# Performance work log

Measured on AMD Instinct MI355X. Metric: run time of the kernel, lower is better.

## Reference

```python
import jax, jax.numpy as jnp
import numpy as np

S, D, H, F = 4096, 1024, 16, 4096
DH = D // H  # 64
EPS = 1e-6


def _layer_norm(x, scale, bias):
    mu = jnp.mean(x, axis=-1, keepdims=True)
    var = jnp.mean(jnp.square(x - mu), axis=-1, keepdims=True)
    return (x - mu) * jax.lax.rsqrt(var + EPS) * scale + bias


def setup_inputs() -> dict:
    key = jax.random.key(0)
    ks = jax.random.split(key, 12)
    s = 0.02
    return {
        "x": jax.random.normal(ks[0], (S, D), jnp.float32),
        "Wq": jax.random.normal(ks[1], (D, H, DH), jnp.float32) * s,
        "bq": jnp.zeros((H, DH), jnp.float32),
        "Wk": jax.random.normal(ks[2], (D, H, DH), jnp.float32) * s,
        "bk": jnp.zeros((H, DH), jnp.float32),
        "Wv": jax.random.normal(ks[3], (D, H, DH), jnp.float32) * s,
        "bv": jnp.zeros((H, DH), jnp.float32),
        "Wo": jax.random.normal(ks[4], (H, DH, D), jnp.float32) * s,
        "bo": jnp.zeros((D,), jnp.float32),
        "ln1_scale": jnp.ones((D,), jnp.float32),
        "ln1_bias": jnp.zeros((D,), jnp.float32),
        "ln2_scale": jnp.ones((D,), jnp.float32),
        "ln2_bias": jnp.zeros((D,), jnp.float32),
        "W1": jax.random.normal(ks[5], (D, F), jnp.float32) * s,
        "b1": jnp.zeros((F,), jnp.float32),
        "W2": jax.random.normal(ks[6], (F, D), jnp.float32) * s,
        "b2": jnp.zeros((D,), jnp.float32),
    }


def reference(x, Wq, bq, Wk, bk, Wv, bv, Wo, bo,
              ln1_scale, ln1_bias, ln2_scale, ln2_bias,
              W1, b1, W2, b2):
    # --- attention block (pre-LN, no mask, no dropout, no RoPE) ---
    y = _layer_norm(x, ln1_scale, ln1_bias)            # [S, D]
    q = jnp.einsum("sd,dhk->shk", y, Wq) + bq          # [S, H, DH]
    k = jnp.einsum("sd,dhk->shk", y, Wk) + bk
    v = jnp.einsum("sd,dhk->shk", y, Wv) + bv
    scale = jnp.float32(1.0 / np.sqrt(DH))
    scores = jnp.einsum("qhd,khd->hqk", q * scale, k)  # [H, S, S]
    w = jax.nn.softmax(scores, axis=-1)
    ctx = jnp.einsum("hqk,khd->qhd", w, v)             # [S, H, DH]
    attn_out = jnp.einsum("qhd,hdo->qo", ctx, Wo) + bo  # [S, D]
    x = x + attn_out
    # --- FFN block ---
    y = _layer_norm(x, ln2_scale, ln2_bias)
    y = jax.nn.gelu(y @ W1 + b1, approximate=False)
    y = y @ W2 + b2
    return x + y
```

## Files before the change

### kernel.cpp

```cpp
#include <hip/hip_runtime.h>
#include <cstdint>
#include <cstddef>


typedef __attribute__((ext_vector_type(8))) __bf16 bf16x8;
typedef __attribute__((ext_vector_type(4))) float f32x4;
typedef __attribute__((ext_vector_type(2))) float f32x2;
typedef __attribute__((ext_vector_type(16))) float f32x16;
typedef __attribute__((ext_vector_type(4))) unsigned int u32x4;

__device__ inline unsigned short f2bf(float f) {
  unsigned int u = __float_as_uint(f);
  u += 0x7fffu + ((u >> 16) & 1u);
  return (unsigned short)(u >> 16);
}

__device__ inline void gload_lds16(const unsigned short* g, unsigned short* l) {
  __builtin_amdgcn_global_load_lds(
      (const __attribute__((address_space(1))) void*)g,
      (__attribute__((address_space(3))) void*)l, 16, 0, 0);
}

__global__ __launch_bounds__(256) void transpose_cvt(const float* __restrict__ in,
                                                     unsigned short* __restrict__ out,
                                                     int K, int N) {
  __shared__ float t[32][33];
  int nb = blockIdx.x * 32, kb = blockIdx.y * 32;
  int tx = threadIdx.x & 31, ty = threadIdx.x >> 5;
#pragma unroll
  for (int i = 0; i < 32; i += 8)
    t[ty + i][tx] = in[(size_t)(kb + ty + i) * N + nb + tx];
  __syncthreads();
#pragma unroll
  for (int i = 0; i < 32; i += 8)
    out[(size_t)(nb + ty + i) * K + kb + tx] = f2bf(t[tx][ty + i]);
}

__global__ __launch_bounds__(256) void concat3(const float* __restrict__ a,
                                               const float* __restrict__ b,
                                               const float* __restrict__ c,
                                               float* __restrict__ out) {
  int i = blockIdx.x * 256 + threadIdx.x;
  float v = (i < 1024) ? a[i] : (i < 2048 ? b[i - 1024] : c[i - 2048]);
  out[i] = v;
}

__global__ __launch_bounds__(256) void ln_kernel(const float* __restrict__ x,
                                                 const float* __restrict__ gamma,
                                                 const float* __restrict__ beta,
                                                 unsigned short* __restrict__ y) {
  int row = blockIdx.x, tid = threadIdx.x;
  const float4 v = ((const float4*)(x + (size_t)row * 1024))[tid];
  float s = v.x + v.y + v.z + v.w;
#pragma unroll
  for (int off = 1; off < 64; off <<= 1) s += __shfl_xor(s, off);
  __shared__ float red1[4], red2[4];
  int wave = tid >> 6;
  if ((tid & 63) == 0) red1[wave] = s;
  __syncthreads();
  float mu = (red1[0] + red1[1] + red1[2] + red1[3]) * (1.0f / 1024.0f);
  float dx = v.x - mu, dy = v.y - mu, dz = v.z - mu, dw = v.w - mu;
  float s2 = dx * dx + dy * dy + dz * dz + dw * dw;
#pragma unroll
  for (int off = 1; off < 64; off <<= 1) s2 += __shfl_xor(s2, off);
  if ((tid & 63) == 0) red2[wave] = s2;
  __syncthreads();
  float var = (red2[0] + red2[1] + red2[2] + red2[3]) * (1.0f / 1024.0f);
  float inv = rsqrtf(var + 1e-6f);
  int c = tid * 4;
  ushort4 o;
  o.x = f2bf(dx * inv * gamma[c + 0] + beta[c + 0]);
  o.y = f2bf(dy * inv * gamma[c + 1] + beta[c + 1]);
  o.z = f2bf(dz * inv * gamma[c + 2] + beta[c + 2]);
  o.w = f2bf(dw * inv * gamma[c + 3] + beta[c + 3]);
  ((ushort4*)(y + (size_t)row * 1024))[tid] = o;
}

template <bool GELU, bool RES, bool OUTBF, bool SCALEQ>
__global__ __launch_bounds__(512, 2) void gemm8(
    const unsigned short* __restrict__ A,
    const unsigned short* __restrict__ BT,
    const float* __restrict__ bias,
    const float* __restrict__ res,
    void* __restrict__ out,
    int M, int N, int K) {
  constexpr int SLOT = 512 * 64;
  __shared__ unsigned short lds[2 * SLOT];
  (void)M;

  const int nbn = N / 256;
  const int bid = blockIdx.x;
  const int cpx = (int)gridDim.x >> 3;
  const int swzb = (bid & 7) * cpx + (bid >> 3);
  const int bm = swzb / nbn, bn = swzb % nbn;
  const int tid = threadIdx.x;
  const int lane = tid & 63, quad = lane >> 4, l16 = lane & 15;
  const int wm = tid >> 8, wn = (tid >> 6) & 3;

  const int rs = tid >> 3;
  const int xo = ((tid & 7) ^ (rs & 7)) * 8;
  const unsigned short* aSrc = A + (size_t)(bm * 256 + rs) * K + xo;
  const unsigned short* bSrc = BT + (size_t)(bn * 256 + rs) * K + xo;

  const int sw0 = (quad ^ (l16 & 7)) * 8;
  const int sw1 = ((quad ^ 4) ^ (l16 & 7)) * 8;
  const int aBase = (wm * 128 + l16) * 64;
  const int bBase = 16384 + (wn * 64 + l16) * 64;

  f32x4 acc[8][4];
  const f32x4 z4 = {0.f, 0.f, 0.f, 0.f};
#pragma unroll
  for (int i = 0; i < 8; ++i)
#pragma unroll
    for (int n = 0; n < 4; ++n) acc[i][n] = z4;

  const int NT = K >> 6;
  {
    unsigned short* dA = lds + (size_t)tid * 8;
    unsigned short* dB = lds + 16384 + (size_t)tid * 8;
#pragma unroll
    for (int u = 0; u < 4; ++u) gload_lds16(aSrc + (size_t)u * 64 * K, dA + u * 4096);
#pragma unroll
    for (int u = 0; u < 4; ++u) gload_lds16(bSrc + (size_t)u * 64 * K, dB + u * 4096);
  }

  for (int j = 0; j < NT; ++j) {
    const int s = j & 1;
    asm volatile("s_waitcnt vmcnt(0) lgkmcnt(0)" ::: "memory");
    __builtin_amdgcn_s_barrier();
    __builtin_amdgcn_sched_barrier(0);
    const unsigned short* Ts = lds + s * SLOT;
    unsigned short* stA = lds + (s ^ 1) * SLOT + (size_t)tid * 8;
    unsigned short* stB = stA + 16384;
    const bool pre = (j + 1 < NT);
    const int kN = (j + 1) << 6;

    bf16x8 af[4][2], bfr[4][2];
#pragma unroll
    for (int mm = 0; mm < 4; ++mm) {
      af[mm][0] = *(const bf16x8*)(Ts + aBase + mm * 1024 + sw0);
      af[mm][1] = *(const bf16x8*)(Ts + aBase + mm * 1024 + sw1);
    }
#pragma unroll
    for (int nn = 0; nn < 2; ++nn) {
      bfr[nn][0] = *(const bf16x8*)(Ts + bBase + nn * 1024 + sw0);
      bfr[nn][1] = *(const bf16x8*)(Ts + bBase + nn * 1024 + sw1);
    }
    if (pre) {
#pragma unroll
      for (int u = 0; u < 4; ++u)
        gload_lds16(aSrc + (size_t)u * 64 * K + kN, stA + u * 4096);
#pragma unroll
      for (int u = 0; u < 4; ++u)
        gload_lds16(bSrc + (size_t)u * 64 * K + kN, stB + u * 4096);
    }
    __builtin_amdgcn_s_barrier();
    __builtin_amdgcn_s_setprio(1);
#pragma unroll
    for (int mm = 0; mm < 4; ++mm)
#pragma unroll
      for (int nn = 0; nn < 2; ++nn) {
        acc[mm][nn] = __builtin_amdgcn_mfma_f32_16x16x32_bf16(af[mm][0], bfr[nn][0], acc[mm][nn], 0, 0, 0);
        acc[mm][nn] = __builtin_amdgcn_mfma_f32_16x16x32_bf16(af[mm][1], bfr[nn][1], acc[mm][nn], 0, 0, 0);
      }
    __builtin_amdgcn_s_setprio(0);
#pragma unroll
    for (int nn = 2; nn < 4; ++nn) {
      bfr[nn][0] = *(const bf16x8*)(Ts + bBase + nn * 1024 + sw0);
      bfr[nn][1] = *(const bf16x8*)(Ts + bBase + nn * 1024 + sw1);
    }
    __builtin_amdgcn_s_barrier();
    __builtin_amdgcn_s_setprio(1);
#pragma unroll
    for (int mm = 0; mm < 4; ++mm)
#pragma unroll
      for (int nn = 2; nn < 4; ++nn) {
        acc[mm][nn] = __builtin_amdgcn_mfma_f32_16x16x32_bf16(af[mm][0], bfr[nn][0], acc[mm][nn], 0, 0, 0);
        acc[mm][nn] = __builtin_amdgcn_mfma_f32_16x16x32_bf16(af[mm][1], bfr[nn][1], acc[mm][nn], 0, 0, 0);
      }
    __builtin_amdgcn_s_setprio(0);
#pragma unroll
    for (int mm = 0; mm < 4; ++mm) {
      af[mm][0] = *(const bf16x8*)(Ts + aBase + 4096 + mm * 1024 + sw0);
      af[mm][1] = *(const bf16x8*)(Ts + aBase + 4096 + mm * 1024 + sw1);
    }
    __builtin_amdgcn_s_barrier();
    __builtin_amdgcn_s_setprio(1);
#pragma unroll
    for (int mm = 0; mm < 4; ++mm)
#pragma unroll
      for (int nn = 0; nn < 2; ++nn) {
        acc[4 + mm][nn] = __builtin_amdgcn_mfma_f32_16x16x32_bf16(af[mm][0], bfr[nn][0], acc[4 + mm][nn], 0, 0, 0);
        acc[4 + mm][nn] = __builtin_amdgcn_mfma_f32_16x16x32_bf16(af[mm][1], bfr[nn][1], acc[4 + mm][nn], 0, 0, 0);
      }
    __builtin_amdgcn_s_setprio(0);
    __builtin_amdgcn_s_barrier();
    __builtin_amdgcn_s_setprio(1);
#pragma unroll
    for (int mm = 0; mm < 4; ++mm)
#pragma unroll
      for (int nn = 2; nn < 4; ++nn) {
        acc[4 + mm][nn] = __builtin_amdgcn_mfma_f32_16x16x32_bf16(af[mm][0], bfr[nn][0], acc[4 + mm][nn], 0, 0, 0);
        acc[4 + mm][nn] = __builtin_amdgcn_mfma_f32_16x16x32_bf16(af[mm][1], bfr[nn][1], acc[4 + mm][nn], 0, 0, 0);
      }
    __builtin_amdgcn_s_setprio(0);
  }

#pragma unroll
  for (int mi = 0; mi < 8; ++mi) {
    const int row0 = bm * 256 + wm * 128 + mi * 16 + quad * 4;
#pragma unroll
    for (int ni = 0; ni < 4; ++ni) {
      const int col = bn * 256 + wn * 64 + ni * 16 + l16;
      const float bv = bias[col];
      const float qs = (SCALEQ && col < 1024) ? 0.18033688f : 1.0f;
#pragma unroll
      for (int r = 0; r < 4; ++r) {
        float v = (acc[mi][ni][r] + bv) * qs;
        if (GELU) v = 0.5f * v * (1.0f + erff(v * 0.70710678118654752440f));
        if (RES) v += res[(size_t)(row0 + r) * N + col];
        if (OUTBF)
          ((unsigned short*)out)[(size_t)(row0 + r) * N + col] = f2bf(v);
        else
          ((float*)out)[(size_t)(row0 + r) * N + col] = v;
      }
    }
  }
}

template <bool GELU, bool RES, bool OUTBF>
__global__ __launch_bounds__(512, 2) void gemm3s(
    const unsigned short* __restrict__ A,
    const unsigned short* __restrict__ BT,
    const float* __restrict__ bias,
    const float* __restrict__ res,
    void* __restrict__ out,
    int M, int N, int K) {
  constexpr int SLOT = 256 * 64;
  __shared__ unsigned short lds[3 * SLOT];
  (void)M;

  const int nbn = N / 128;
  const int bid = blockIdx.x;
  const int cpx = (int)gridDim.x >> 3;
  const int swzb = (bid & 7) * cpx + (bid >> 3);
  const int bm = swzb / nbn, bn = swzb % nbn;
  const int tid = threadIdx.x;
  const int lane = tid & 63, quad = lane >> 4, l16 = lane & 15;
  const int wm = tid >> 8, wn = (tid >> 6) & 3;

  const int rs = tid >> 3;
  const int xo = ((tid & 7) ^ (rs & 7)) * 8;
  const unsigned short* aSrc = A + (size_t)(bm * 128 + rs) * K + xo;
  const unsigned short* bSrc = BT + (size_t)(bn * 128 + rs) * K + xo;

  const int sw0 = (quad ^ (l16 & 7)) * 8;
  const int sw1 = ((quad ^ 4) ^ (l16 & 7)) * 8;
  const int aBase = (wm * 64 + l16) * 64;
  const int bBase = 8192 + (wn * 32 + l16) * 64;

  f32x4 acc[4][2];
  const f32x4 z4 = {0.f, 0.f, 0.f, 0.f};
#pragma unroll
  for (int i = 0; i < 4; ++i)
#pragma unroll
    for (int n = 0; n < 2; ++n) acc[i][n] = z4;

  const int NT = K >> 6;
  {
    unsigned short* d0 = lds + (size_t)tid * 8;
    gload_lds16(aSrc, d0);
    gload_lds16(aSrc + (size_t)64 * K, d0 + 4096);
    gload_lds16(bSrc, d0 + 8192);
    gload_lds16(bSrc + (size_t)64 * K, d0 + 8192 + 4096);
    if (NT > 1) {
      unsigned short* d1 = lds + SLOT + (size_t)tid * 8;
      gload_lds16(aSrc + 64, d1);
      gload_lds16(aSrc + (size_t)64 * K + 64, d1 + 4096);
      gload_lds16(bSrc + 64, d1 + 8192);
      gload_lds16(bSrc + (size_t)64 * K + 64, d1 + 8192 + 4096);
    }
  }

  int sl = 0;
  for (int j = 0; j < NT; ++j) {
    if (j + 1 < NT)
      asm volatile("s_waitcnt vmcnt(4) lgkmcnt(0)" ::: "memory");
    else
      asm volatile("s_waitcnt vmcnt(0) lgkmcnt(0)" ::: "memory");
    __builtin_amdgcn_s_barrier();
    __builtin_amdgcn_sched_barrier(0);
    const unsigned short* Ts = lds + sl * SLOT;
    const int sl2 = (sl >= 1) ? sl - 1 : 2;
    unsigned short* st = lds + sl2 * SLOT + (size_t)tid * 8;

    bf16x8 af[2][2], bfr[2][2];
#pragma unroll
    for (int mm = 0; mm < 2; ++mm) {
      af[mm][0] = *(const bf16x8*)(Ts + aBase + mm * 1024 + sw0);
      af[mm][1] = *(const bf16x8*)(Ts + aBase + mm * 1024 + sw1);
    }
#pragma unroll
    for (int nn = 0; nn < 2; ++nn) {
      bfr[nn][0] = *(const bf16x8*)(Ts + bBase + nn * 1024 + sw0);
      bfr[nn][1] = *(const bf16x8*)(Ts + bBase + nn * 1024 + sw1);
    }
    if (j + 2 < NT) {
      const int kN = (j + 2) << 6;
      gload_lds16(aSrc + kN, st);
      gload_lds16(aSrc + (size_t)64 * K + kN, st + 4096);
      gload_lds16(bSrc + kN, st + 8192);
      gload_lds16(bSrc + (size_t)64 * K + kN, st + 8192 + 4096);
    }
    __builtin_amdgcn_s_barrier();
    __builtin_amdgcn_s_setprio(1);
#pragma unroll
    for (int mm = 0; mm < 2; ++mm)
#pragma unroll
      for (int nn = 0; nn < 2; ++nn) {
        acc[mm][nn] = __builtin_amdgcn_mfma_f32_16x16x32_bf16(af[mm][0], bfr[nn][0], acc[mm][nn], 0, 0, 0);
        acc[mm][nn] = __builtin_amdgcn_mfma_f32_16x16x32_bf16(af[mm][1], bfr[nn][1], acc[mm][nn], 0, 0, 0);
      }
    __builtin_amdgcn_s_setprio(0);
#pragma unroll
    for (int mm = 0; mm < 2; ++mm) {
      af[mm][0] = *(const bf16x8*)(Ts + aBase + 2048 + mm * 1024 + sw0);
      af[mm][1] = *(const bf16x8*)(Ts + aBase + 2048 + mm * 1024 + sw1);
    }
    __builtin_amdgcn_s_barrier();
    __builtin_amdgcn_s_setprio(1);
#pragma unroll
    for (int mm = 0; mm < 2; ++mm)
#pragma unroll
      for (int nn = 0; nn < 2; ++nn) {
        acc[2 + mm][nn] = __builtin_amdgcn_mfma_f32_16x16x32_bf16(af[mm][0], bfr[nn][0], acc[2 + mm][nn], 0, 0, 0);
        acc[2 + mm][nn] = __builtin_amdgcn_mfma_f32_16x16x32_bf16(af[mm][1], bfr[nn][1], acc[2 + mm][nn], 0, 0, 0);
      }
    __builtin_amdgcn_s_setprio(0);
    sl = (sl == 2) ? 0 : sl + 1;
  }

#pragma unroll
  for (int mi = 0; mi < 4; ++mi) {
    const int row0 = bm * 128 + wm * 64 + mi * 16 + quad * 4;
#pragma unroll
    for (int ni = 0; ni < 2; ++ni) {
      const int col = bn * 128 + wn * 32 + ni * 16 + l16;
      const float bv = bias[col];
#pragma unroll
      for (int r = 0; r < 4; ++r) {
        float v = acc[mi][ni][r] + bv;
        if (GELU) v = 0.5f * v * (1.0f + erff(v * 0.70710678118654752440f));
        if (RES) v += res[(size_t)(row0 + r) * N + col];
        if (OUTBF)
          ((unsigned short*)out)[(size_t)(row0 + r) * N + col] = f2bf(v);
        else
          ((float*)out)[(size_t)(row0 + r) * N + col] = v;
      }
    }
  }
}

__global__ __launch_bounds__(256) void prep_kv(const unsigned short* __restrict__ qkv,
                                               unsigned short* __restrict__ Kp,
                                               unsigned short* __restrict__ Vp) {
  __shared__ unsigned short Vt[64 * 64];
  int t = blockIdx.x, h = blockIdx.y;
  int tid = threadIdx.x;
  const int r2 = tid >> 3, c0 = (tid & 7) * 8;
  size_t tb = ((size_t)h * 64 + t) * 4096;
  {
    const unsigned short* kp = qkv + (size_t)(t * 64 + r2) * 3072 + 1024 + h * 64 + c0;
    uint4 k0 = *(const uint4*)kp;
    uint4 k1 = *(const uint4*)(kp + (size_t)32 * 3072);
    int c = c0 >> 3;
    *(uint4*)(Kp + tb + c * 512 + r2 * 8) = k0;
    *(uint4*)(Kp + tb + c * 512 + (r2 + 32) * 8) = k1;
  }
  {
    const unsigned short* vp = qkv + (size_t)(t * 64 + 2 * r2) * 3072 + 2048 + h * 64 + c0;
    uint4 v0 = *(const uint4*)vp;
    uint4 v1 = *(const uint4*)(vp + 3072);
    const unsigned short* p0 = (const unsigned short*)&v0;
    const unsigned short* p1 = (const unsigned short*)&v1;
#pragma unroll
    for (int dd = 0; dd < 8; dd++) {
      unsigned int pk = (unsigned int)p0[dd] | ((unsigned int)p1[dd] << 16);
      *(unsigned int*)&Vt[(c0 + dd) * 64 + 2 * r2] = pk;
    }
  }
  __syncthreads();
#pragma unroll
  for (int u0 = 0; u0 < 2; u0++) {
    int u = tid + u0 * 256;
    *(uint4*)(Vp + tb + u * 8) = *(const uint4*)&Vt[(u & 63) * 64 + (u >> 6) * 8];
  }
}

#define ATTN_STEP(KF, VF, KN, VN, T)                                                  \
  {                                                                                   \
    f32x16 accS;                                                                      \
    _Pragma("unroll")                                                                 \
    for (int r = 0; r < 16; r++) accS[r] = 0.f;                                       \
    _Pragma("unroll")                                                                 \
    for (int kk = 0; kk < 4; kk++)                                                    \
      accS = __builtin_amdgcn_mfma_f32_32x32x16_bf16(KF[kk], qf[kk], accS, 0, 0, 0);  \
    if ((T) < 63) {                                                                   \
      const unsigned short* kt = kB + (size_t)((T) + 1) * 4096;                       \
      const unsigned short* vt = vB + (size_t)((T) + 1) * 4096;                       \
      _Pragma("unroll")                                                               \
      for (int kk = 0; kk < 4; kk++) KN[kk] = *(const bf16x8*)(kt + kk * 1024);       \
      VN[0] = *(const bf16x8*)(vt);                                                   \
      VN[1] = *(const bf16x8*)(vt + 1024);                                            \
      VN[2] = *(const bf16x8*)(vt + 256);                                             \
      VN[3] = *(const bf16x8*)(vt + 1024 + 256);                                      \
    }                                                                                 \
    unsigned int pd[8];                                                               \
    _Pragma("unroll")                                                                 \
    for (int i = 0; i < 8; i++) {                                                     \
      float a = __builtin_amdgcn_exp2f(accS[2 * i]);                                  \
      float b = __builtin_amdgcn_exp2f(accS[2 * i + 1]);                              \
      f32x2 ab = {a, b};                                                              \
      lp2 += ab;                                                                      \
      pd[i] = __builtin_amdgcn_perm(__float_as_uint(b), __float_as_uint(a), 0x07060302); \
    }                                                                                 \
    asm("v_permlane32_swap_b32 %0, %1" : "+v"(pd[0]), "+v"(pd[2]));                   \
    asm("v_permlane32_swap_b32 %0, %1" : "+v"(pd[1]), "+v"(pd[3]));                   \
    asm("v_permlane32_swap_b32 %0, %1" : "+v"(pd[4]), "+v"(pd[6]));                   \
    asm("v_permlane32_swap_b32 %0, %1" : "+v"(pd[5]), "+v"(pd[7]));                   \
    u32x4 f0 = {pd[0], pd[1], pd[2], pd[3]};                                          \
    u32x4 f1 = {pd[4], pd[5], pd[6], pd[7]};                                          \
    bf16x8 pa0 = __builtin_bit_cast(bf16x8, f0);                                      \
    bf16x8 pa1 = __builtin_bit_cast(bf16x8, f1);                                      \
    accO0 = __builtin_amdgcn_mfma_f32_32x32x16_bf16(pa0, VF[0], accO0, 0, 0, 0);      \
    accO1 = __builtin_amdgcn_mfma_f32_32x32x16_bf16(pa0, VF[2], accO1, 0, 0, 0);      \
    accO0 = __builtin_amdgcn_mfma_f32_32x32x16_bf16(pa1, VF[1], accO0, 0, 0, 0);      \
    accO1 = __builtin_amdgcn_mfma_f32_32x32x16_bf16(pa1, VF[3], accO1, 0, 0, 0);      \
  }

__global__ __launch_bounds__(256, 3) void attn_kernel(const unsigned short* __restrict__ qkv,
                                                      const unsigned short* __restrict__ Kp,
                                                      const unsigned short* __restrict__ Vp,
                                                      unsigned short* __restrict__ ctx) {
  __shared__ float comb[2 * 32 * 64];
  __shared__ float lpart[4 * 32];
  int qt = blockIdx.x, h = blockIdx.y;
  int tid = threadIdx.x;
  int w = tid >> 6, lane = tid & 63;
  int l31 = lane & 31, hi = lane >> 5;
  int qsub = w & 1, kvh = w >> 1;

  bf16x8 qf[4];
  {
    const unsigned short* qp = qkv + (size_t)(qt * 64 + qsub * 32 + l31) * 3072 + h * 64 + hi * 8;
#pragma unroll
    for (int kk = 0; kk < 4; kk++) qf[kk] = *(const bf16x8*)(qp + kk * 16);
  }

  const size_t hb = (size_t)h * 64 * 4096;
  const unsigned short* kB = Kp + hb + hi * 512 + (kvh * 32 + l31) * 8;
  const unsigned short* vB = Vp + hb + (kvh * 4 + hi) * 512 + l31 * 8;

  f32x16 accO0, accO1;
  f32x2 lp2 = {0.f, 0.f};
#pragma unroll
  for (int r = 0; r < 16; r++) { accO0[r] = 0.f; accO1[r] = 0.f; }

  bf16x8 kfa[4], vfa[4], kfb[4], vfb[4];
#pragma unroll
  for (int kk = 0; kk < 4; kk++) kfa[kk] = *(const bf16x8*)(kB + kk * 1024);
  vfa[0] = *(const bf16x8*)(vB);
  vfa[1] = *(const bf16x8*)(vB + 1024);
  vfa[2] = *(const bf16x8*)(vB + 256);
  vfa[3] = *(const bf16x8*)(vB + 1024 + 256);

  for (int t = 0; t < 64; t += 2) {
    ATTN_STEP(kfa, vfa, kfb, vfb, t);
    ATTN_STEP(kfb, vfb, kfa, vfa, t + 1);
  }

  float lp = lp2.x + lp2.y;
  lp += __shfl_xor(lp, 32);
  if (hi == 0) lpart[(kvh * 2 + qsub) * 32 + l31] = lp;
  if (kvh == 1) {
#pragma unroll
    for (int r = 0; r < 16; r++) {
      int q = (r & 3) + 8 * (r >> 2) + 4 * hi;
      comb[(qsub * 32 + q) * 64 + l31] = accO0[r];
      comb[(qsub * 32 + q) * 64 + 32 + l31] = accO1[r];
    }
  }
  __syncthreads();
  if (kvh == 0) {
#pragma unroll
    for (int r = 0; r < 16; r++) {
      int q = (r & 3) + 8 * (r >> 2) + 4 * hi;
      float l = lpart[qsub * 32 + q] + lpart[(2 + qsub) * 32 + q];
      float inv = 1.0f / l;
      float v0 = (accO0[r] + comb[(qsub * 32 + q) * 64 + l31]) * inv;
      float v1 = (accO1[r] + comb[(qsub * 32 + q) * 64 + 32 + l31]) * inv;
      int row = qt * 64 + qsub * 32 + q;
      size_t o = (size_t)row * 1024 + h * 64;
      ctx[o + l31] = f2bf(v0);
      ctx[o + 32 + l31] = f2bf(v1);
    }
  }
}

extern "C" void kernel_launch(void* const* d_in, const int* in_sizes, int n_in,
                              void* d_out, int out_size, void* d_ws, size_t ws_size,
                              hipStream_t stream) {
  const float* x   = (const float*)d_in[0];
  const float* Wq  = (const float*)d_in[1];
  const float* bq  = (const float*)d_in[2];
  const float* Wk  = (const float*)d_in[3];
  const float* bk  = (const float*)d_in[4];
  const float* Wv  = (const float*)d_in[5];
  const float* bv  = (const float*)d_in[6];
  const float* Wo  = (const float*)d_in[7];
  const float* bo  = (const float*)d_in[8];
  const float* g1  = (const float*)d_in[9];
  const float* be1 = (const float*)d_in[10];
  const float* g2  = (const float*)d_in[11];
  const float* be2 = (const float*)d_in[12];
  const float* W1  = (const float*)d_in[13];
  const float* b1  = (const float*)d_in[14];
  const float* W2  = (const float*)d_in[15];
  const float* b2  = (const float*)d_in[16];
  float* out = (float*)d_out;

  char* p = (char*)d_ws;
  unsigned short* WqkvT = (unsigned short*)p; p += (size_t)3072 * 1024 * 2;
  unsigned short* WoT   = (unsigned short*)p; p += (size_t)1024 * 1024 * 2;
  unsigned short* W1T   = (unsigned short*)p; p += (size_t)4096 * 1024 * 2;
  unsigned short* W2T   = (unsigned short*)p; p += (size_t)1024 * 4096 * 2;
  float*          bqkv  = (float*)p;          p += 16384;
  unsigned short* y1    = (unsigned short*)p; p += (size_t)4096 * 1024 * 2;
  unsigned short* qkvb  = (unsigned short*)p; p += (size_t)4096 * 3072 * 2;
  unsigned short* ctxb  = (unsigned short*)p; p += (size_t)4096 * 1024 * 2;
  float*          x1    = (float*)p;          p += (size_t)4096 * 1024 * 4;
  unsigned short* Kp    = (unsigned short*)p; p += (size_t)16 * 64 * 4096 * 2;
  unsigned short* Vp    = (unsigned short*)p; p += (size_t)16 * 64 * 4096 * 2;
  unsigned short* hbuf  = qkvb;

  dim3 b256(256);
  dim3 b512(512);
  transpose_cvt<<<dim3(32, 32), b256, 0, stream>>>(Wq, WqkvT, 1024, 1024);
  transpose_cvt<<<dim3(32, 32), b256, 0, stream>>>(Wk, WqkvT + (size_t)1024 * 1024, 1024, 1024);
  transpose_cvt<<<dim3(32, 32), b256, 0, stream>>>(Wv, WqkvT + (size_t)2048 * 1024, 1024, 1024);
  transpose_cvt<<<dim3(32, 32), b256, 0, stream>>>(Wo, WoT, 1024, 1024);
  transpose_cvt<<<dim3(128, 32), b256, 0, stream>>>(W1, W1T, 1024, 4096);
  transpose_cvt<<<dim3(32, 128), b256, 0, stream>>>(W2, W2T, 4096, 1024);
  concat3<<<12, b256, 0, stream>>>(bq, bk, bv, bqkv);

  ln_kernel<<<4096, b256, 0, stream>>>(x, g1, be1, y1);
  gemm8<false, false, true, true><<<dim3(192), b512, 0, stream>>>(y1, WqkvT, bqkv, nullptr, qkvb, 4096, 3072, 1024);
  prep_kv<<<dim3(64, 16), b256, 0, stream>>>(qkvb, Kp, Vp);
  attn_kernel<<<dim3(64, 16), b256, 0, stream>>>(qkvb, Kp, Vp, ctxb);
  gemm3s<false, true, false><<<dim3(256), b512, 0, stream>>>(ctxb, WoT, bo, x, x1, 4096, 1024, 1024);
  ln_kernel<<<4096, b256, 0, stream>>>(x1, g2, be2, y1);
  gemm8<true, false, true, false><<<dim3(256), b512, 0, stream>>>(y1, W1T, b1, nullptr, hbuf, 4096, 4096, 1024);
  gemm3s<false, true, false><<<dim3(256), b512, 0, stream>>>(hbuf, W2T, b2, x1, out, 4096, 1024, 4096);
}
```

Before: 383.6 us.

## Merge weight-prep launches into one kernel and simplify attention K/V prefetch

Replaces the six transpose launches and the bias concat with a single prep_all kernel that picks its source matrix from the block index, removing per-launch overhead and tail gaps between small kernels. Separately, the attention loop drops the double-buffered K/V register macro. It now loads V at the top of each iteration and prefetches only the next K, which lowers register pressure but exposes V load latency before the PV MFMAs.

```diff
diff --git a/kernel.cpp b/kernel.cpp
--- a/kernel.cpp
+++ b/kernel.cpp
@@ -21,12 +21,38 @@
       (__attribute__((address_space(3))) void*)l, 16, 0, 0);
 }
 
-__global__ __launch_bounds__(256) void transpose_cvt(const float* __restrict__ in,
-                                                     unsigned short* __restrict__ out,
-                                                     int K, int N) {
+__global__ __launch_bounds__(256) void prep_all(
+    const float* __restrict__ Wq, const float* __restrict__ Wk,
+    const float* __restrict__ Wv, const float* __restrict__ Wo,
+    const float* __restrict__ W1, const float* __restrict__ W2,
+    const float* __restrict__ bq, const float* __restrict__ bk,
+    const float* __restrict__ bv,
+    unsigned short* __restrict__ WqkvT, unsigned short* __restrict__ WoT,
+    unsigned short* __restrict__ W1T, unsigned short* __restrict__ W2T,
+    float* __restrict__ bqkv) {
+  int b = blockIdx.x;
+  if (b < 12) {
+    int i = b * 256 + threadIdx.x;
+    bqkv[i] = (i < 1024) ? bq[i] : (i < 2048 ? bk[i - 1024] : bv[i - 2048]);
+    return;
+  }
+  b -= 12;
+  const float* in;
+  unsigned short* out;
+  int K, N, nbx;
+  if (b < 4096) {
+    const int sel = b >> 10;
+    in = (sel == 0) ? Wq : (sel == 1) ? Wk : (sel == 2) ? Wv : Wo;
+    out = (sel == 3) ? WoT : WqkvT + (size_t)sel * 1024 * 1024;
+    K = 1024; N = 1024; nbx = 32; b &= 1023;
+  } else if (b < 8192) {
+    b -= 4096; in = W1; out = W1T; K = 1024; N = 4096; nbx = 128;
+  } else {
+    b -= 8192; in = W2; out = W2T; K = 4096; N = 1024; nbx = 32;
+  }
+  const int nb = (b % nbx) * 32, kb = (b / nbx) * 32;
   __shared__ float t[32][33];
-  int nb = blockIdx.x * 32, kb = blockIdx.y * 32;
-  int tx = threadIdx.x & 31, ty = threadIdx.x >> 5;
+  const int tx = threadIdx.x & 31, ty = threadIdx.x >> 5;
 #pragma unroll
   for (int i = 0; i < 32; i += 8)
     t[ty + i][tx] = in[(size_t)(kb + ty + i) * N + nb + tx];
@@ -34,15 +60,6 @@
 #pragma unroll
   for (int i = 0; i < 32; i += 8)
     out[(size_t)(nb + ty + i) * K + kb + tx] = f2bf(t[tx][ty + i]);
-}
-
-__global__ __launch_bounds__(256) void concat3(const float* __restrict__ a,
-                                               const float* __restrict__ b,
-                                               const float* __restrict__ c,
-                                               float* __restrict__ out) {
-  int i = blockIdx.x * 256 + threadIdx.x;
-  float v = (i < 1024) ? a[i] : (i < 2048 ? b[i - 1024] : c[i - 2048]);
-  out[i] = v;
 }
 
 __global__ __launch_bounds__(256) void ln_kernel(const float* __restrict__ x,
@@ -397,47 +414,6 @@
   }
 }
 
-#define ATTN_STEP(KF, VF, KN, VN, T)                                                  \
-  {                                                                                   \
-    f32x16 accS;                                                                      \
-    _Pragma("unroll")                                                                 \
-    for (int r = 0; r < 16; r++) accS[r] = 0.f;                                       \
-    _Pragma("unroll")                                                                 \
-    for (int kk = 0; kk < 4; kk++)                                                    \
-      accS = __builtin_amdgcn_mfma_f32_32x32x16_bf16(KF[kk], qf[kk], accS, 0, 0, 0);  \
-    if ((T) < 63) {                                                                   \
-      const unsigned short* kt = kB + (size_t)((T) + 1) * 4096;                       \
-      const unsigned short* vt = vB + (size_t)((T) + 1) * 4096;                       \
-      _Pragma("unroll")                                                               \
-      for (int kk = 0; kk < 4; kk++) KN[kk] = *(const bf16x8*)(kt + kk * 1024);       \
-      VN[0] = *(const bf16x8*)(vt);                                                   \
-      VN[1] = *(const bf16x8*)(vt + 1024);                                            \
-      VN[2] = *(const bf16x8*)(vt + 256);                                             \
-      VN[3] = *(const bf16x8*)(vt + 1024 + 256);                                      \
-    }                                                                                 \
-    unsigned int pd[8];                                                               \
-    _Pragma("unroll")                                                                 \
-    for (int i = 0; i < 8; i++) {                                                     \
-      float a = __builtin_amdgcn_exp2f(accS[2 * i]);                                  \
-      float b = __builtin_amdgcn_exp2f(accS[2 * i + 1]);                              \
-      f32x2 ab = {a, b};                                                              \
-      lp2 += ab;                                                                      \
-      pd[i] = __builtin_amdgcn_perm(__float_as_uint(b), __float_as_uint(a), 0x07060302); \
-    }                                                                                 \
-    asm("v_permlane32_swap_b32 %0, %1" : "+v"(pd[0]), "+v"(pd[2]));                   \
-    asm("v_permlane32_swap_b32 %0, %1" : "+v"(pd[1]), "+v"(pd[3]));                   \
-    asm("v_permlane32_swap_b32 %0, %1" : "+v"(pd[4]), "+v"(pd[6]));                   \
-    asm("v_permlane32_swap_b32 %0, %1" : "+v"(pd[5]), "+v"(pd[7]));                   \
-    u32x4 f0 = {pd[0], pd[1], pd[2], pd[3]};                                          \
-    u32x4 f1 = {pd[4], pd[5], pd[6], pd[7]};                                          \
-    bf16x8 pa0 = __builtin_bit_cast(bf16x8, f0);                                      \
-    bf16x8 pa1 = __builtin_bit_cast(bf16x8, f1);                                      \
-    accO0 = __builtin_amdgcn_mfma_f32_32x32x16_bf16(pa0, VF[0], accO0, 0, 0, 0);      \
-    accO1 = __builtin_amdgcn_mfma_f32_32x32x16_bf16(pa0, VF[2], accO1, 0, 0, 0);      \
-    accO0 = __builtin_amdgcn_mfma_f32_32x32x16_bf16(pa1, VF[1], accO0, 0, 0, 0);      \
-    accO1 = __builtin_amdgcn_mfma_f32_32x32x16_bf16(pa1, VF[3], accO1, 0, 0, 0);      \
-  }
-
 __global__ __launch_bounds__(256, 3) void attn_kernel(const unsigned short* __restrict__ qkv,
                                                       const unsigned short* __restrict__ Kp,
                                                       const unsigned short* __restrict__ Vp,
@@ -466,17 +442,52 @@
 #pragma unroll
   for (int r = 0; r < 16; r++) { accO0[r] = 0.f; accO1[r] = 0.f; }
 
-  bf16x8 kfa[4], vfa[4], kfb[4], vfb[4];
-#pragma unroll
-  for (int kk = 0; kk < 4; kk++) kfa[kk] = *(const bf16x8*)(kB + kk * 1024);
-  vfa[0] = *(const bf16x8*)(vB);
-  vfa[1] = *(const bf16x8*)(vB + 1024);
-  vfa[2] = *(const bf16x8*)(vB + 256);
-  vfa[3] = *(const bf16x8*)(vB + 1024 + 256);
-
-  for (int t = 0; t < 64; t += 2) {
-    ATTN_STEP(kfa, vfa, kfb, vfb, t);
-    ATTN_STEP(kfb, vfb, kfa, vfa, t + 1);
+  bf16x8 kf[4];
+#pragma unroll
+  for (int kk = 0; kk < 4; kk++) kf[kk] = *(const bf16x8*)(kB + kk * 1024);
+
+  for (int t = 0; t < 64; t++) {
+    const unsigned short* vt = vB + (size_t)t * 4096;
+    bf16x8 vA0 = *(const bf16x8*)(vt);
+    bf16x8 vA1 = *(const bf16x8*)(vt + 1024);
+    bf16x8 vB0 = *(const bf16x8*)(vt + 256);
+    bf16x8 vB1 = *(const bf16x8*)(vt + 1024 + 256);
+
+    f32x16 accS;
+#pragma unroll
+    for (int r = 0; r < 16; r++) accS[r] = 0.f;
+#pragma unroll
+    for (int kk = 0; kk < 4; kk++)
+      accS = __builtin_amdgcn_mfma_f32_32x32x16_bf16(kf[kk], qf[kk], accS, 0, 0, 0);
+
+    if (t < 63) {
+      const unsigned short* kt = kB + (size_t)(t + 1) * 4096;
+#pragma unroll
+      for (int kk = 0; kk < 4; kk++) kf[kk] = *(const bf16x8*)(kt + kk * 1024);
+    }
+
+    unsigned int pd[8];
+#pragma unroll
+    for (int i = 0; i < 8; i++) {
+      float a = __builtin_amdgcn_exp2f(accS[2 * i]);
+      float b = __builtin_amdgcn_exp2f(accS[2 * i + 1]);
+      f32x2 ab = {a, b};
+      lp2 += ab;
+      pd[i] = __builtin_amdgcn_perm(__float_as_uint(b), __float_as_uint(a), 0x07060302);
+    }
+    asm("v_permlane32_swap_b32 %0, %1" : "+v"(pd[0]), "+v"(pd[2]));
+    asm("v_permlane32_swap_b32 %0, %1" : "+v"(pd[1]), "+v"(pd[3]));
+    asm("v_permlane32_swap_b32 %0, %1" : "+v"(pd[4]), "+v"(pd[6]));
+    asm("v_permlane32_swap_b32 %0, %1" : "+v"(pd[5]), "+v"(pd[7]));
+    u32x4 f0 = {pd[0], pd[1], pd[2], pd[3]};
+    u32x4 f1 = {pd[4], pd[5], pd[6], pd[7]};
+    bf16x8 pa0 = __builtin_bit_cast(bf16x8, f0);
+    bf16x8 pa1 = __builtin_bit_cast(bf16x8, f1);
+
+    accO0 = __builtin_amdgcn_mfma_f32_32x32x16_bf16(pa0, vA0, accO0, 0, 0, 0);
+    accO1 = __builtin_amdgcn_mfma_f32_32x32x16_bf16(pa0, vB0, accO1, 0, 0, 0);
+    accO0 = __builtin_amdgcn_mfma_f32_32x32x16_bf16(pa1, vA1, accO0, 0, 0, 0);
+    accO1 = __builtin_amdgcn_mfma_f32_32x32x16_bf16(pa1, vB1, accO1, 0, 0, 0);
   }
 
   float lp = lp2.x + lp2.y;
@@ -545,13 +556,8 @@
 
   dim3 b256(256);
   dim3 b512(512);
-  transpose_cvt<<<dim3(32, 32), b256, 0, stream>>>(Wq, WqkvT, 1024, 1024);
-  transpose_cvt<<<dim3(32, 32), b256, 0, stream>>>(Wk, WqkvT + (size_t)1024 * 1024, 1024, 1024);
-  transpose_cvt<<<dim3(32, 32), b256, 0, stream>>>(Wv, WqkvT + (size_t)2048 * 1024, 1024, 1024);
-  transpose_cvt<<<dim3(32, 32), b256, 0, stream>>>(Wo, WoT, 1024, 1024);
-  transpose_cvt<<<dim3(128, 32), b256, 0, stream>>>(W1, W1T, 1024, 4096);
-  transpose_cvt<<<dim3(32, 128), b256, 0, stream>>>(W2, W2T, 4096, 1024);
-  concat3<<<12, b256, 0, stream>>>(bq, bk, bv, bqkv);
+  prep_all<<<dim3(12300), b256, 0, stream>>>(Wq, Wk, Wv, Wo, W1, W2, bq, bk, bv,
+                                             WqkvT, WoT, W1T, W2T, bqkv);
 
   ln_kernel<<<4096, b256, 0, stream>>>(x, g1, be1, y1);
   gemm8<false, false, true, true><<<dim3(192), b512, 0, stream>>>(y1, WqkvT, bqkv, nullptr, qkvb, 4096, 3072, 1024);
```

Measured after the change: 367.5 us. 4.2% less time.
